# Performance work log

Measured on AMD Instinct MI355X. Metric: run time of the kernel, lower is better.

Reference implementation:

```python
import jax, jax.numpy as jnp
import numpy as np

N_COLS = 107
CAT_SLICES = [(1, 10), (10, 26), (27, 34), (34, 49), (49, 55), (55, 60), (60, 62), (65, 107)]
MSE_COLS = [0, 26, 62, 63, 64]
BATCH = 524288


def setup_inputs() -> dict:
    key = jax.random.key(0)
    k_dec, k_cont, k_cat = jax.random.split(key, 3)
    data_decoded = jax.random.normal(k_dec, (BATCH, N_COLS), dtype=jnp.float32)
    # Build data_true: continuous cols random, categorical slices exactly one-hot.
    data_true = jax.random.uniform(k_cont, (BATCH, N_COLS), dtype=jnp.float32)
    rows = jnp.arange(BATCH)
    for i, (s, e) in enumerate(CAT_SLICES):
        kk = jax.random.fold_in(k_cat, i)
        labels = jax.random.randint(kk, (BATCH,), 0, e - s)
        data_true = data_true.at[:, s:e].set(0.0)
        data_true = data_true.at[rows, s + labels].set(1.0)
    return {"data_decoded": data_decoded, "data_true": data_true, "batch_size": BATCH}


def _ce(logits, onehot_true):
    # torch nonzero()[:,1] on an exact one-hot slice == argmax
    labels = jnp.argmax(onehot_true, axis=1)
    logp = jax.nn.log_softmax(logits, axis=1)
    return -jnp.mean(jnp.take_along_axis(logp, labels[:, None], axis=1))


def _mse(a, b):
    d = a - b
    return jnp.mean(d * d)


def reference(data_decoded, data_true, batch_size):
    mse_loss = jnp.float32(0.0)
    for c in MSE_COLS:
        mse_loss = mse_loss + _mse(data_decoded[:, c], data_true[:, c])
    ce_loss = jnp.float32(0.0)
    for s, e in CAT_SLICES:
        ce_loss = ce_loss + _ce(data_decoded[:, s:e], data_true[:, s:e])
    multi_loss = mse_loss + ce_loss
    return multi_loss, mse_loss, ce_loss
```

## Files before the change

kernel.cpp:

```cpp
#include <hip/hip_runtime.h>

#define NCOLS 107
#define ROWS_PER_GROUP 4
#define GROUP_F4 NCOLS
#define THREADS 256
#define BN 4
#define NBAT 27

typedef float f4 __attribute__((ext_vector_type(4)));

__device__ __host__ __forceinline__ constexpr int bstart(int b) { return b * BN; }
__device__ __host__ __forceinline__ constexpr int blen(int b) {
    return b < NBAT - 1 ? BN : (GROUP_F4 - BN * (NBAT - 1));
}

__device__ __host__ __forceinline__ constexpr int slice_of(int col) {
    return (col >= 1  && col < 10) ? 0 :
           (col >= 10 && col < 26) ? 1 :
           (col >= 27 && col < 34) ? 2 :
           (col >= 34 && col < 49) ? 3 :
           (col >= 49 && col < 55) ? 4 :
           (col >= 55 && col < 60) ? 5 :
           (col >= 60 && col < 62) ? 6 :
           (col >= 65)             ? 7 : -1;
}
__device__ __host__ __forceinline__ constexpr int slice_last(int sid) {
    return sid == 0 ?  9 : sid == 1 ? 25 : sid == 2 ? 33 : sid == 3 ? 48 :
           sid == 4 ? 54 : sid == 5 ? 59 : sid == 6 ? 61 : 106;
}

template<int L>
__device__ __forceinline__ void elem(float d, float t, float (&s)[8],
                                     float& mse, float& dot, float& lse) {
    constexpr int col = L % NCOLS;
    constexpr int sid = slice_of(col);
    if constexpr (sid < 0) {
        float df = d - t;
        mse += df * df;
    } else {
        s[sid] += __expf(d);
        dot = __builtin_fmaf(d, t, dot);
        if constexpr (col == slice_last(sid)) {
            lse += __logf(s[sid]);
            s[sid] = 0.0f;
        }
    }
}


template<int B, int K = 0>
__device__ __forceinline__ void bload(const f4* __restrict__ gd,
                                      const f4* __restrict__ gt,
                                      f4 (&d)[BN], f4 (&t)[BN]) {
    if constexpr (K < blen(B)) {
        d[K] = gd[bstart(B) + K];
        t[K] = gt[bstart(B) + K];
        bload<B, K + 1>(gd, gt, d, t);
    }
}

template<int B, int K = 0>
__device__ __forceinline__ void bproc(const f4 (&d)[BN], const f4 (&t)[BN],
                                      float (&s)[8],
                                      float& mse, float& dot, float& lse) {
    if constexpr (K < blen(B)) {
        constexpr int C = bstart(B) + K;
        elem<4 * C + 0>(d[K][0], t[K][0], s, mse, dot, lse);
        elem<4 * C + 1>(d[K][1], t[K][1], s, mse, dot, lse);
        elem<4 * C + 2>(d[K][2], t[K][2], s, mse, dot, lse);
        elem<4 * C + 3>(d[K][3], t[K][3], s, mse, dot, lse);
        bproc<B, K + 1>(d, t, s, mse, dot, lse);
    }
}

template<int B>
__device__ __forceinline__ void stage(const f4* __restrict__ gd,
                                      const f4* __restrict__ gt,
                                      f4 (&d0)[BN], f4 (&t0)[BN],
                                      f4 (&d1)[BN], f4 (&t1)[BN],
                                      f4 (&d2)[BN], f4 (&t2)[BN],
                                      float (&s)[8],
                                      float& mse, float& dot, float& lse) {
    f4 d3[BN], t3[BN];
    if constexpr (B + 3 < NBAT) {
        bload<B + 3>(gd, gt, d3, t3);
        __builtin_amdgcn_sched_barrier(0);
    }
    bproc<B>(d0, t0, s, mse, dot, lse);
    if constexpr (B + 1 < NBAT) {
        stage<B + 1>(gd, gt, d1, t1, d2, t2, d3, t3, s, mse, dot, lse);
    }
}

__global__ __launch_bounds__(THREADS, 2) void multiloss_main(
        const float* __restrict__ dec, const float* __restrict__ tru,
        float2* __restrict__ ws, int ngroups) {
    int g = blockIdx.x * THREADS + threadIdx.x;
    float mse = 0.0f, dot = 0.0f, lse = 0.0f;
    float s[8] = {0.0f, 0.0f, 0.0f, 0.0f, 0.0f, 0.0f, 0.0f, 0.0f};
    if (g < ngroups) {
        const f4* gd = (const f4*)dec + (size_t)g * GROUP_F4;
        const f4* gt = (const f4*)tru + (size_t)g * GROUP_F4;
        f4 ad[BN], at[BN], bd[BN], bt[BN], cd[BN], ct[BN];
        bload<0>(gd, gt, ad, at);
        bload<1>(gd, gt, bd, bt);
        bload<2>(gd, gt, cd, ct);
        stage<0>(gd, gt, ad, at, bd, bt, cd, ct, s, mse, dot, lse);
    }
    float ce = lse - dot;
#pragma unroll
    for (int off = 32; off > 0; off >>= 1) {
        mse += __shfl_down(mse, off, 64);
        ce  += __shfl_down(ce,  off, 64);
    }
    int lane  = threadIdx.x & 63;
    int gwave = (blockIdx.x * THREADS + threadIdx.x) >> 6;
    if (lane == 0)
        ws[gwave] = make_float2(mse, ce);
}

__global__ __launch_bounds__(256) void multiloss_fin(
        const float2* __restrict__ ws, float* __restrict__ out,
        int nslots, float invN) {
    float m = 0.0f, c = 0.0f;
    for (int i = threadIdx.x; i < nslots; i += 256) {
        float2 v = ws[i];
        m += v.x; c += v.y;
    }
#pragma unroll
    for (int off = 32; off > 0; off >>= 1) {
        m += __shfl_down(m, off, 64);
        c += __shfl_down(c, off, 64);
    }
    __shared__ float sm[4], sc[4];
    int wid  = threadIdx.x >> 6;
    int lane = threadIdx.x & 63;
    if (lane == 0) { sm[wid] = m; sc[wid] = c; }
    __syncthreads();
    if (threadIdx.x == 0) {
        float mse = (sm[0] + sm[1] + sm[2] + sm[3]) * invN;
        float ce  = (sc[0] + sc[1] + sc[2] + sc[3]) * invN;
        out[0] = mse + ce;
        out[1] = mse;
        out[2] = ce;
    }
}

extern "C" void kernel_launch(void* const* d_in, const int* in_sizes, int n_in,
                              void* d_out, int out_size, void* d_ws, size_t ws_size,
                              hipStream_t stream) {
    const float* dec = (const float*)d_in[0];
    const float* tru = (const float*)d_in[1];
    int nrows   = in_sizes[0] / NCOLS;
    int ngroups = nrows / ROWS_PER_GROUP;
    int nblocks = (ngroups + THREADS - 1) / THREADS;
    int nwaves  = nblocks * (THREADS / 64);
    float2* ws = (float2*)d_ws;
    multiloss_main<<<nblocks, THREADS, 0, stream>>>(dec, tru, ws, ngroups);
    multiloss_fin<<<1, 256, 0, stream>>>(ws, (float*)d_out, nwaves,
                                         1.0f / (float)nrows);
}
```

Measured before the change: 463.8 us.

## Split each row group across two threads with LDS merge of straddling softmax

Each 4-row group, which one thread used to process alone, is now split between two threads in different waves. One thread takes the first 54 float4s and the other the remaining 53. The categorical slice that straddles the split has its partial exp-sum passed through shared memory and combined after a block barrier. This halves the per-thread serial work and raises occupancy (launch bounds go from 2 to 4), aiming to hide memory latency better. The cost is a __syncthreads per block and the assumption that the group count divides evenly by 128, since the bounds check was removed.

```diff
diff --git a/kernel.cpp b/kernel.cpp
--- a/kernel.cpp
+++ b/kernel.cpp
@@ -1,17 +1,18 @@
 #include <hip/hip_runtime.h>
 
 #define NCOLS 107
-#define ROWS_PER_GROUP 4
-#define GROUP_F4 NCOLS
+#define GROUP_F4 107
 #define THREADS 256
 #define BN 4
-#define NBAT 27
+#define GROUPS_PER_BLOCK 128
 
 typedef float f4 __attribute__((ext_vector_type(4)));
 
-__device__ __host__ __forceinline__ constexpr int bstart(int b) { return b * BN; }
-__device__ __host__ __forceinline__ constexpr int blen(int b) {
-    return b < NBAT - 1 ? BN : (GROUP_F4 - BN * (NBAT - 1));
+__device__ __host__ __forceinline__ constexpr int nbat(int cnt) {
+    return (cnt + BN - 1) / BN;
+}
+__device__ __host__ __forceinline__ constexpr int blen(int b, int cnt) {
+    return (BN * (b + 1) <= cnt) ? BN : (cnt - BN * b);
 }
 
 __device__ __host__ __forceinline__ constexpr int slice_of(int col) {
@@ -31,10 +32,17 @@
 
 template<int L>
 __device__ __forceinline__ void elem(float d, float t, float (&s)[8],
-                                     float& mse, float& dot, float& lse) {
+                                     float& mse, float& dot, float& lse,
+                                     float& hs, float& ts) {
     constexpr int col = L % NCOLS;
     constexpr int sid = slice_of(col);
-    if constexpr (sid < 0) {
+    if constexpr (L == 215) {
+        hs += __expf(d);
+        dot = __builtin_fmaf(d, t, dot);
+    } else if constexpr (L >= 216 && L <= 223) {
+        ts += __expf(d);
+        dot = __builtin_fmaf(d, t, dot);
+    } else if constexpr (sid < 0) {
         float df = d - t;
         mse += df * df;
     } else {
@@ -47,76 +55,96 @@
     }
 }
 
-
-template<int B, int K = 0>
+template<int C0, int CNT, int B, int K = 0>
 __device__ __forceinline__ void bload(const f4* __restrict__ gd,
                                       const f4* __restrict__ gt,
                                       f4 (&d)[BN], f4 (&t)[BN]) {
-    if constexpr (K < blen(B)) {
-        d[K] = gd[bstart(B) + K];
-        t[K] = gt[bstart(B) + K];
-        bload<B, K + 1>(gd, gt, d, t);
+    if constexpr (K < blen(B, CNT)) {
+        d[K] = gd[C0 + B * BN + K];
+        t[K] = gt[C0 + B * BN + K];
+        bload<C0, CNT, B, K + 1>(gd, gt, d, t);
     }
 }
 
-template<int B, int K = 0>
+template<int C0, int CNT, int B, int K = 0>
 __device__ __forceinline__ void bproc(const f4 (&d)[BN], const f4 (&t)[BN],
-                                      float (&s)[8],
-                                      float& mse, float& dot, float& lse) {
-    if constexpr (K < blen(B)) {
-        constexpr int C = bstart(B) + K;
-        elem<4 * C + 0>(d[K][0], t[K][0], s, mse, dot, lse);
-        elem<4 * C + 1>(d[K][1], t[K][1], s, mse, dot, lse);
-        elem<4 * C + 2>(d[K][2], t[K][2], s, mse, dot, lse);
-        elem<4 * C + 3>(d[K][3], t[K][3], s, mse, dot, lse);
-        bproc<B, K + 1>(d, t, s, mse, dot, lse);
+                                      float (&s)[8], float& mse, float& dot,
+                                      float& lse, float& hs, float& ts) {
+    if constexpr (K < blen(B, CNT)) {
+        constexpr int C = C0 + B * BN + K;
+        elem<4 * C + 0>(d[K][0], t[K][0], s, mse, dot, lse, hs, ts);
+        elem<4 * C + 1>(d[K][1], t[K][1], s, mse, dot, lse, hs, ts);
+        elem<4 * C + 2>(d[K][2], t[K][2], s, mse, dot, lse, hs, ts);
+        elem<4 * C + 3>(d[K][3], t[K][3], s, mse, dot, lse, hs, ts);
+        bproc<C0, CNT, B, K + 1>(d, t, s, mse, dot, lse, hs, ts);
     }
 }
 
-template<int B>
+template<int C0, int CNT, int B>
 __device__ __forceinline__ void stage(const f4* __restrict__ gd,
                                       const f4* __restrict__ gt,
                                       f4 (&d0)[BN], f4 (&t0)[BN],
                                       f4 (&d1)[BN], f4 (&t1)[BN],
                                       f4 (&d2)[BN], f4 (&t2)[BN],
-                                      float (&s)[8],
-                                      float& mse, float& dot, float& lse) {
+                                      float (&s)[8], float& mse, float& dot,
+                                      float& lse, float& hs, float& ts) {
     f4 d3[BN], t3[BN];
-    if constexpr (B + 3 < NBAT) {
-        bload<B + 3>(gd, gt, d3, t3);
+    if constexpr (B + 3 < nbat(CNT)) {
+        bload<C0, CNT, B + 3>(gd, gt, d3, t3);
         __builtin_amdgcn_sched_barrier(0);
     }
-    bproc<B>(d0, t0, s, mse, dot, lse);
-    if constexpr (B + 1 < NBAT) {
-        stage<B + 1>(gd, gt, d1, t1, d2, t2, d3, t3, s, mse, dot, lse);
+    bproc<C0, CNT, B>(d0, t0, s, mse, dot, lse, hs, ts);
+    if constexpr (B + 1 < nbat(CNT)) {
+        stage<C0, CNT, B + 1>(gd, gt, d1, t1, d2, t2, d3, t3,
+                              s, mse, dot, lse, hs, ts);
     }
 }
 
-__global__ __launch_bounds__(THREADS, 2) void multiloss_main(
+template<int C0, int CNT>
+__device__ __forceinline__ void run(const f4* __restrict__ gd,
+                                    const f4* __restrict__ gt,
+                                    float (&s)[8], float& mse, float& dot,
+                                    float& lse, float& hs, float& ts) {
+    f4 ad[BN], at[BN], bd[BN], bt[BN], cd[BN], ct[BN];
+    bload<C0, CNT, 0>(gd, gt, ad, at);
+    bload<C0, CNT, 1>(gd, gt, bd, bt);
+    bload<C0, CNT, 2>(gd, gt, cd, ct);
+    stage<C0, CNT, 0>(gd, gt, ad, at, bd, bt, cd, ct, s, mse, dot, lse, hs, ts);
+}
+
+__global__ __launch_bounds__(THREADS, 4) void multiloss_main(
         const float* __restrict__ dec, const float* __restrict__ tru,
-        float2* __restrict__ ws, int ngroups) {
-    int g = blockIdx.x * THREADS + threadIdx.x;
-    float mse = 0.0f, dot = 0.0f, lse = 0.0f;
+        float2* __restrict__ ws) {
+    __shared__ float headlds[GROUPS_PER_BLOCK];
+    int lane = threadIdx.x & 63;
+    int wid  = threadIdx.x >> 6;
+    int half = wid >> 1;
+    int gloc = (wid & 1) * 64 + lane;
+    int g    = blockIdx.x * GROUPS_PER_BLOCK + gloc;
+
+    float mse = 0.0f, dot = 0.0f, lse = 0.0f, hs = 0.0f, ts = 0.0f;
     float s[8] = {0.0f, 0.0f, 0.0f, 0.0f, 0.0f, 0.0f, 0.0f, 0.0f};
-    if (g < ngroups) {
-        const f4* gd = (const f4*)dec + (size_t)g * GROUP_F4;
-        const f4* gt = (const f4*)tru + (size_t)g * GROUP_F4;
-        f4 ad[BN], at[BN], bd[BN], bt[BN], cd[BN], ct[BN];
-        bload<0>(gd, gt, ad, at);
-        bload<1>(gd, gt, bd, bt);
-        bload<2>(gd, gt, cd, ct);
-        stage<0>(gd, gt, ad, at, bd, bt, cd, ct, s, mse, dot, lse);
+    const f4* gd = (const f4*)dec + (size_t)g * GROUP_F4;
+    const f4* gt = (const f4*)tru + (size_t)g * GROUP_F4;
+
+    if (half == 0) {
+        run<0, 54>(gd, gt, s, mse, dot, lse, hs, ts);
+        headlds[gloc] = hs;
+    } else {
+        run<54, 53>(gd, gt, s, mse, dot, lse, hs, ts);
     }
+    __syncthreads();
+    if (half == 1)
+        lse += __logf(headlds[gloc] + ts);
+
     float ce = lse - dot;
 #pragma unroll
     for (int off = 32; off > 0; off >>= 1) {
         mse += __shfl_down(mse, off, 64);
         ce  += __shfl_down(ce,  off, 64);
     }
-    int lane  = threadIdx.x & 63;
-    int gwave = (blockIdx.x * THREADS + threadIdx.x) >> 6;
     if (lane == 0)
-        ws[gwave] = make_float2(mse, ce);
+        ws[blockIdx.x * 4 + wid] = make_float2(mse, ce);
 }
 
 __global__ __launch_bounds__(256) void multiloss_fin(
@@ -152,11 +180,11 @@
     const float* dec = (const float*)d_in[0];
     const float* tru = (const float*)d_in[1];
     int nrows   = in_sizes[0] / NCOLS;
-    int ngroups = nrows / ROWS_PER_GROUP;
-    int nblocks = (ngroups + THREADS - 1) / THREADS;
-    int nwaves  = nblocks * (THREADS / 64);
+    int ngroups = nrows / 4;
+    int nblocks = ngroups / GROUPS_PER_BLOCK;
+    int nwaves  = nblocks * 4;
     float2* ws = (float2*)d_ws;
-    multiloss_main<<<nblocks, THREADS, 0, stream>>>(dec, tru, ws, ngroups);
+    multiloss_main<<<nblocks, THREADS, 0, stream>>>(dec, tru, ws);
     multiloss_fin<<<1, 256, 0, stream>>>(ws, (float*)d_out, nwaves,
                                          1.0f / (float)nrows);
 }
```

After: 528.6 us. 14.0% more time.
